# Performance work log

Measured on AMD Instinct MI355X. Metric: run time of the kernel, lower is better.

## Reference

```python
import jax, jax.numpy as jnp
import numpy as np

EMBED_DIM = 1024

def setup_inputs() -> dict:
    key = jax.random.key(0)
    kx, kwq, kbq, kwk, kbk, kwv, kbv = jax.random.split(key, 7)
    d = EMBED_DIM
    s = 1.0 / np.sqrt(d)
    x = jax.random.normal(kx, (4, 2048, d), dtype=jnp.float32)
    # nn.Linear weights are [out, in]; we store transposed [in, out] for x @ W
    Wq = jax.random.uniform(kwq, (d, d), jnp.float32, -s, s)
    bq = jax.random.uniform(kbq, (d,), jnp.float32, -s, s)
    Wk = jax.random.uniform(kwk, (d, d), jnp.float32, -s, s)
    bk = jax.random.uniform(kbk, (d,), jnp.float32, -s, s)
    Wv = jax.random.uniform(kwv, (d, d), jnp.float32, -s, s)
    bv = jax.random.uniform(kbv, (d,), jnp.float32, -s, s)
    return {"x": x, "Wq": Wq, "bq": bq, "Wk": Wk, "bk": bk, "Wv": Wv, "bv": bv}

def reference(x, Wq, bq, Wk, bk, Wv, bv):
    d = x.shape[-1]
    q = x @ Wq + bq            # [B, S, D]
    k = x @ Wk + bk            # [B, S, D]
    v = x @ Wv + bv            # [B, S, D]
    scores = jnp.einsum('bsd,btd->bst', q, k) / jnp.sqrt(jnp.asarray(d, x.dtype))
    attn = jax.nn.softmax(scores, axis=-1)  # [B, S, S]
    return jnp.einsum('bst,btd->bsd', attn, v)
```

## Files before the change

kernel.cpp:

```cpp
#include <hip/hip_runtime.h>
#include <hip/hip_bf16.h>
#include <stdint.h>


typedef short bf16x8 __attribute__((ext_vector_type(8)));
typedef float f32x4 __attribute__((ext_vector_type(4)));
typedef unsigned short us4 __attribute__((ext_vector_type(4)));
typedef unsigned short us8 __attribute__((ext_vector_type(8)));
typedef _Float16 h8v __attribute__((ext_vector_type(8)));
typedef unsigned short us;

#define B_ 4
#define S_ 2048
#define D_ 1024

__device__ __forceinline__ us f2bf(float f) {
  unsigned int u = __float_as_uint(f);
  unsigned int r = (u + 0x7fffu + ((u >> 16) & 1u)) >> 16;
  return (us)r;
}

__device__ __forceinline__ void gl2lds16(void* lds, const void* g) {
  __builtin_amdgcn_global_load_lds(
      (const __attribute__((address_space(1))) unsigned int*)(uintptr_t)g,
      (__attribute__((address_space(3))) unsigned int*)(uintptr_t)lds,
      16, 0, 0);
}

__device__ __forceinline__ void sched_fence() { __builtin_amdgcn_sched_barrier(0); }
__device__ __forceinline__ void barrier_f() {
  sched_fence(); __builtin_amdgcn_s_barrier(); sched_fence();
}

template<int BM, int R0, int R1>
__device__ __forceinline__ void stageR(us* buf, const us* gA, size_t sA,
                                       const us* gB, size_t sB,
                                       int wave, int lane) {
  int slot = ((lane & 7) ^ (lane >> 3)) << 4;
  char* l = (char*)buf;
#pragma unroll
  for (int r = R0; r < R1; ++r) {
    int row = r * 64 + wave * 8 + (lane >> 3);
    const char* src;
    if (r * 64 < BM)
      src = (const char*)gA + (size_t)row * sA + slot;
    else
      src = (const char*)gB + (size_t)(row - BM) * sB + slot;
    gl2lds16(l + r * 8192 + wave * 1024, src);
  }
}

template<int EPI, int BM, int BN, int WNS>
__global__ __launch_bounds__(512, 2) void gemm8p(
    const us* __restrict__ Aall, const us* __restrict__ Ball,
    size_t aBatch, size_t bBatch, int sAe, int sBe, int nt,
    const float* __restrict__ bq, const float* __restrict__ bk,
    const float* __restrict__ bv, void* __restrict__ outp,
    us* __restrict__ vtb) {
  __shared__ __align__(16) us lds[3][(BM + BN) * 64];
  int tid = threadIdx.x, lane = tid & 63, wave = tid >> 6;
  int wm = wave / WNS, wn = wave % WNS;
  int m0 = blockIdx.x * BM, n0 = blockIdx.y * BN;
  size_t bz = blockIdx.z;
  const us* gA = Aall + bz * aBatch + (size_t)m0 * sAe;
  const us* gB = Ball + bz * bBatch + (size_t)n0 * sBe;
  size_t sA = (size_t)sAe * 2, sB = (size_t)sBe * 2;

  stageR<BM, 0, 6>(lds[0], gA, sA, gB, sB, wave, lane);
  stageR<BM, 0, 6>(lds[1], gA + 64, sA, gB + 64, sB, wave, lane);

  int r15 = lane & 15, kg = lane >> 4, l7 = lane & 7;
  int x0 = (kg ^ l7) << 4;
  f32x4 acc[4][4] = {};

  for (int t = 0; t < nt; ++t) {
    if (t == nt - 1) asm volatile("s_waitcnt vmcnt(0)" ::: "memory");
    else             asm volatile("s_waitcnt vmcnt(6)" ::: "memory");
    barrier_f();
    const us* buf = lds[t % 3];
    us* nbuf = (us*)lds[(t + 2) % 3];
    bool dostage = (t + 2 < nt);
    const us* gA2 = gA + (size_t)(t + 2) * 64;
    const us* gB2 = gB + (size_t)(t + 2) * 64;
    const char* pa = (const char*)buf + (size_t)(wm * 64 + r15) * 128;
    const char* pb = (const char*)buf + (size_t)(BM + wn * 64 + r15) * 128;

    if (dostage) stageR<BM, 0, 3>(nbuf, gA2, sA, gB2, sB, wave, lane);
    bf16x8 A0[4], B0[4];
#pragma unroll
    for (int f = 0; f < 4; ++f) A0[f] = *(const bf16x8*)(pa + f * 2048 + x0);
#pragma unroll
    for (int f = 0; f < 4; ++f) B0[f] = *(const bf16x8*)(pb + f * 2048 + x0);
    __builtin_amdgcn_s_setprio(1);
#pragma unroll
    for (int fn = 0; fn < 4; ++fn)
#pragma unroll
      for (int fm = 0; fm < 4; ++fm)
        acc[fm][fn] = __builtin_amdgcn_mfma_f32_16x16x32_bf16(A0[fm], B0[fn], acc[fm][fn], 0, 0, 0);
    __builtin_amdgcn_s_setprio(0);

    if (dostage) stageR<BM, 3, 6>(nbuf, gA2, sA, gB2, sB, wave, lane);
    bf16x8 A1[4], B1[4];
#pragma unroll
    for (int f = 0; f < 4; ++f) A1[f] = *(const bf16x8*)(pa + f * 2048 + (x0 ^ 64));
#pragma unroll
    for (int f = 0; f < 4; ++f) B1[f] = *(const bf16x8*)(pb + f * 2048 + (x0 ^ 64));
    __builtin_amdgcn_s_setprio(1);
#pragma unroll
    for (int fn = 0; fn < 4; ++fn)
#pragma unroll
      for (int fm = 0; fm < 4; ++fm)
        acc[fm][fn] = __builtin_amdgcn_mfma_f32_16x16x32_bf16(A1[fm], B1[fn], acc[fm][fn], 0, 0, 0);
    __builtin_amdgcn_s_setprio(0);
  }

#pragma unroll
  for (int fm = 0; fm < 4; ++fm)
#pragma unroll
    for (int fn = 0; fn < 4; ++fn) {
      int col = n0 + wn * 64 + fn * 16 + r15;
      int row0 = m0 + wm * 64 + fm * 16 + ((lane >> 4) << 2);
      if constexpr (EPI == 0) {
        int mat = col >> 10;
        const float* bp = (mat == 0) ? bq : (mat == 1) ? bk : bv;
        float bb = bp[col & 1023];
        if (mat < 2) {
          us* ob = (us*)outp + ((size_t)mat << 23);
#pragma unroll
          for (int r = 0; r < 4; ++r)
            ob[(size_t)(row0 + r) * D_ + (col & 1023)] = f2bf(acc[fm][fn][r] + bb);
        } else {
          int b = row0 >> 11, trow = row0 & 2047, dcol = col & 1023;
          us4 v4 = {f2bf(acc[fm][fn][0] + bb), f2bf(acc[fm][fn][1] + bb),
                    f2bf(acc[fm][fn][2] + bb), f2bf(acc[fm][fn][3] + bb)};
          *(us4*)(vtb + (size_t)b * D_ * S_ + (size_t)dcol * S_ + trow) = v4;
        }
      } else {
        float* ob = (float*)outp + bz * (size_t)(S_ * D_);
#pragma unroll
        for (int r = 0; r < 4; ++r)
          ob[(size_t)(row0 + r) * D_ + col] = acc[fm][fn][r];
      }
    }
}

__global__ __launch_bounds__(512, 2) void s2k(
    const us* __restrict__ Aall, const us* __restrict__ Ball,
    _Float16* __restrict__ scores) {
  __shared__ __align__(16) us lds3[3][16384];
  const int tid = threadIdx.x, lane = tid & 63, wave = tid >> 6;
  const int wm = wave >> 2, wn = wave & 3;
  const int m0 = blockIdx.x * 256, n0 = blockIdx.y * 256;
  const size_t bz = blockIdx.z;
  const char* gA = (const char*)(Aall + bz * (size_t)(S_ * D_) + (size_t)m0 * D_);
  const char* gB = (const char*)(Ball + bz * (size_t)(S_ * D_) + (size_t)n0 * D_);
  const size_t sA = (size_t)D_ * 2, sB = (size_t)D_ * 2;
  const int nt = 32;

  const int r15 = lane & 15, kg = lane >> 4;
  const int srcslot = (((lane & 3) ^ ((lane >> 3) & 3)) << 4);
  const int srow = wave * 16 + (lane >> 2);

  auto stage = [&](int bi, int t) {
    char* l = (char*)lds3[bi];
    const size_t koff = (size_t)t * 64;
#pragma unroll
    for (int r = 0; r < 4; ++r) {
      int row = r * 128 + srow;
      const char* src = (row < 256)
          ? gA + (size_t)row * sA + koff + srcslot
          : gB + (size_t)(row - 256) * sB + koff + srcslot;
      gl2lds16(l + r * 8192 + wave * 1024, src);
    }
  };

  stage(0, 0);
  stage(1, 1);

  f32x4 acc[8][4] = {};
  for (int t = 0; t < nt; ++t) {
    if (t == nt - 1) asm volatile("s_waitcnt vmcnt(0)" ::: "memory");
    else             asm volatile("s_waitcnt vmcnt(4)" ::: "memory");
    barrier_f();
    if (t + 2 < nt) stage((t + 2) % 3, t + 2);
    const char* buf = (const char*)lds3[t % 3];

    bf16x8 Af[8], Bf[4];
#pragma unroll
    for (int f = 0; f < 8; ++f) {
      int tr = wm * 128 + f * 16 + r15;
      Af[f] = *(const bf16x8*)(buf + tr * 64 + ((kg ^ ((tr >> 1) & 3)) << 4));
    }
#pragma unroll
    for (int n = 0; n < 4; ++n) {
      int tr = 256 + wn * 64 + n * 16 + r15;
      Bf[n] = *(const bf16x8*)(buf + tr * 64 + ((kg ^ ((tr >> 1) & 3)) << 4));
    }
    __builtin_amdgcn_s_setprio(1);
#pragma unroll
    for (int n = 0; n < 4; ++n)
#pragma unroll
      for (int f = 0; f < 8; ++f)
        acc[f][n] = __builtin_amdgcn_mfma_f32_16x16x32_bf16(Af[f], Bf[n], acc[f][n], 0, 0, 0);
    __builtin_amdgcn_s_setprio(0);
  }

  _Float16* sc = scores + bz * (size_t)(S_ * S_);
#pragma unroll
  for (int fm = 0; fm < 8; ++fm)
#pragma unroll
    for (int fn = 0; fn < 4; ++fn) {
      int col = n0 + wn * 64 + fn * 16 + r15;
      int row0 = m0 + wm * 128 + fm * 16 + ((lane >> 4) << 2);
#pragma unroll
      for (int r = 0; r < 4; ++r)
        sc[(size_t)(row0 + r) * S_ + col] = (_Float16)(acc[fm][fn][r] * 0.03125f);
    }
}

__global__ __launch_bounds__(256) void wt_prep(const float* __restrict__ Wq,
                                               const float* __restrict__ Wk,
                                               const float* __restrict__ Wv,
                                               us* __restrict__ wtb) {
  __shared__ us hs[64][65];
  int mat = blockIdx.z;
  const float* W = (mat == 0) ? Wq : (mat == 1) ? Wk : Wv;
  int n0 = blockIdx.x * 64, k0 = blockIdx.y * 64;
  int tid = threadIdx.x;
#pragma unroll
  for (int i = 0; i < 16; ++i) {
    int idx = tid + i * 256;
    int r = idx >> 6, c = idx & 63;
    hs[r][c] = f2bf(W[(size_t)(k0 + r) * D_ + (n0 + c)]);
  }
  __syncthreads();
  us* o = wtb + ((size_t)mat << 20);
#pragma unroll
  for (int i = 0; i < 16; ++i) {
    int idx = tid + i * 256;
    int r = idx >> 6, c = idx & 63;
    o[(size_t)(n0 + r) * D_ + (k0 + c)] = hs[c][r];
  }
}

__global__ __launch_bounds__(256) void xcast(const float* __restrict__ x,
                                             us* __restrict__ xb) {
  size_t i = ((size_t)blockIdx.x * 256 + threadIdx.x) * 8;
  float4 f0 = *(const float4*)(x + i);
  float4 f1 = *(const float4*)(x + i + 4);
  float vals[8] = {f0.x, f0.y, f0.z, f0.w, f1.x, f1.y, f1.z, f1.w};
  union { bf16x8 v; us s_[8]; } H;
#pragma unroll
  for (int e = 0; e < 8; ++e) H.s_[e] = f2bf(vals[e]);
  *(bf16x8*)(xb + i) = H.v;
}

__global__ __launch_bounds__(256) void softmax_k(const _Float16* __restrict__ scores,
                                                 us* __restrict__ pb) {
  int row = blockIdx.x, tid = threadIdx.x, lane = tid & 63, wave = tid >> 6;
  const _Float16* s = scores + (size_t)row * S_;
  h8v a8 = *(const h8v*)(s + tid * 8);
  float a[8];
#pragma unroll
  for (int e = 0; e < 8; ++e) a[e] = (float)a8[e];
  float m = a[0];
#pragma unroll
  for (int e = 1; e < 8; ++e) m = fmaxf(m, a[e]);
#pragma unroll
  for (int o = 32; o; o >>= 1) m = fmaxf(m, __shfl_xor(m, o));
  __shared__ float red[4];
  if (lane == 0) red[wave] = m;
  __syncthreads();
  m = fmaxf(fmaxf(red[0], red[1]), fmaxf(red[2], red[3]));
  float p[8];
  float sum = 0.f;
#pragma unroll
  for (int e = 0; e < 8; ++e) { p[e] = expf(a[e] - m); sum += p[e]; }
#pragma unroll
  for (int o = 32; o; o >>= 1) sum += __shfl_xor(sum, o);
  __syncthreads();
  if (lane == 0) red[wave] = sum;
  __syncthreads();
  float inv = 1.0f / (red[0] + red[1] + red[2] + red[3]);
  us8 h;
#pragma unroll
  for (int e = 0; e < 8; ++e) h[e] = f2bf(p[e] * inv);
  *(us8*)(pb + (size_t)row * S_ + tid * 8) = h;
}

extern "C" void kernel_launch(void* const* d_in, const int* in_sizes, int n_in,
                              void* d_out, int out_size, void* d_ws, size_t ws_size,
                              hipStream_t stream) {
  const float* x  = (const float*)d_in[0];
  const float* Wq = (const float*)d_in[1];
  const float* bq = (const float*)d_in[2];
  const float* Wk = (const float*)d_in[3];
  const float* bk = (const float*)d_in[4];
  const float* Wv = (const float*)d_in[5];
  const float* bv = (const float*)d_in[6];
  float* out = (float*)d_out;
  char* ws = (char*)d_ws;
  const size_t MB = 1024 * 1024;
  us* qb   = (us*)(ws + 0 * MB);
  us* kb   = (us*)(ws + 16 * MB);
  us* vtb  = (us*)(ws + 32 * MB);
  us* wtb  = (us*)(ws + 48 * MB);
  us* xb   = (us*)(ws + 54 * MB);
  _Float16* scores = (_Float16*)(ws + 70 * MB);
  us* pb   = (us*)(ws + 102 * MB);

  wt_prep<<<dim3(16, 16, 3), 256, 0, stream>>>(Wq, Wk, Wv, wtb);
  xcast<<<dim3(4096), 256, 0, stream>>>(x, xb);
  gemm8p<0, 128, 256, 4><<<dim3(64, 12, 1), 512, 0, stream>>>(
      xb, wtb, 0, 0, D_, D_, 16, bq, bk, bv, qb, vtb);
  s2k<<<dim3(8, 8, 4), 512, 0, stream>>>(qb, kb, scores);
  softmax_k<<<dim3(B_ * S_), 256, 0, stream>>>(scores, pb);
  gemm8p<2, 256, 128, 2><<<dim3(8, 8, 4), 512, 0, stream>>>(
      pb, vtb, (size_t)S_ * S_, (size_t)D_ * S_, S_, S_, 32,
      nullptr, nullptr, nullptr, out, nullptr);
}
```

Measured before the change: 152.2 us.

## Fold Q and K projections into a single precomputed Wq·Wkᵀ matrix

Rewrites the scores as (x·Wq·Wkᵀ)·xᵀ plus a per-key bias c = x·(Wk·bq). Terms that are constant along a softmax row are dropped, because softmax ignores them. This removes one of the three 8192x1024x1024 projection GEMMs: one GEMM now produces E = x·M alongside the transposed V. The cost is several new small kernels: a naive MFMA product forming M from global memory, a matrix-vector pass for u, and a pass re-reading fp32 x to build c. It also adds extra bf16 rounding from storing M in bf16.

```diff
diff --git a/kernel.cpp b/kernel.cpp
--- a/kernel.cpp
+++ b/kernel.cpp
@@ -54,8 +54,7 @@
 __global__ __launch_bounds__(512, 2) void gemm8p(
     const us* __restrict__ Aall, const us* __restrict__ Ball,
     size_t aBatch, size_t bBatch, int sAe, int sBe, int nt,
-    const float* __restrict__ bq, const float* __restrict__ bk,
-    const float* __restrict__ bv, void* __restrict__ outp,
+    const float* __restrict__ bias1, void* __restrict__ outp,
     us* __restrict__ vtb) {
   __shared__ __align__(16) us lds[3][(BM + BN) * 64];
   int tid = threadIdx.x, lane = tid & 63, wave = tid >> 6;
@@ -120,16 +119,15 @@
     for (int fn = 0; fn < 4; ++fn) {
       int col = n0 + wn * 64 + fn * 16 + r15;
       int row0 = m0 + wm * 64 + fm * 16 + ((lane >> 4) << 2);
-      if constexpr (EPI == 0) {
+      if constexpr (EPI == 3) {
         int mat = col >> 10;
-        const float* bp = (mat == 0) ? bq : (mat == 1) ? bk : bv;
-        float bb = bp[col & 1023];
-        if (mat < 2) {
-          us* ob = (us*)outp + ((size_t)mat << 23);
+        if (mat == 0) {
+          us* ob = (us*)outp;
 #pragma unroll
           for (int r = 0; r < 4; ++r)
-            ob[(size_t)(row0 + r) * D_ + (col & 1023)] = f2bf(acc[fm][fn][r] + bb);
+            ob[(size_t)(row0 + r) * D_ + col] = f2bf(acc[fm][fn][r]);
         } else {
+          float bb = bias1[col & 1023];
           int b = row0 >> 11, trow = row0 & 2047, dcol = col & 1023;
           us4 v4 = {f2bf(acc[fm][fn][0] + bb), f2bf(acc[fm][fn][1] + bb),
                     f2bf(acc[fm][fn][2] + bb), f2bf(acc[fm][fn][3] + bb)};
@@ -146,7 +144,7 @@
 
 __global__ __launch_bounds__(512, 2) void s2k(
     const us* __restrict__ Aall, const us* __restrict__ Ball,
-    _Float16* __restrict__ scores) {
+    const float* __restrict__ cvp, _Float16* __restrict__ scores) {
   __shared__ __align__(16) us lds3[3][16384];
   const int tid = threadIdx.x, lane = tid & 63, wave = tid >> 6;
   const int wm = wave >> 2, wn = wave & 3;
@@ -206,25 +204,97 @@
   }
 
   _Float16* sc = scores + bz * (size_t)(S_ * S_);
+  const float* cb = cvp + bz * (size_t)S_;
 #pragma unroll
   for (int fm = 0; fm < 8; ++fm)
 #pragma unroll
     for (int fn = 0; fn < 4; ++fn) {
       int col = n0 + wn * 64 + fn * 16 + r15;
       int row0 = m0 + wm * 128 + fm * 16 + ((lane >> 4) << 2);
+      float cv = cb[col];
 #pragma unroll
       for (int r = 0; r < 4; ++r)
-        sc[(size_t)(row0 + r) * S_ + col] = (_Float16)(acc[fm][fn][r] * 0.03125f);
-    }
-}
-
-__global__ __launch_bounds__(256) void wt_prep(const float* __restrict__ Wq,
-                                               const float* __restrict__ Wk,
-                                               const float* __restrict__ Wv,
-                                               us* __restrict__ wtb) {
+        sc[(size_t)(row0 + r) * S_ + col] = (_Float16)((acc[fm][fn][r] + cv) * 0.03125f);
+    }
+}
+
+__global__ __launch_bounds__(256) void mprep(const us* __restrict__ wkb,
+                                             const us* __restrict__ wqb,
+                                             us* __restrict__ mtb) {
+  int tid = threadIdx.x, lane = tid & 63, wave = tid >> 6;
+  int j0 = blockIdx.x * 64, i0 = blockIdx.y * 64;
+  int r15 = lane & 15, kg = lane >> 4;
+  f32x4 acc[4] = {};
+  for (int kk = 0; kk < D_; kk += 32) {
+    bf16x8 a = *(const bf16x8*)(wkb + (size_t)(j0 + wave * 16 + r15) * D_ + kk + kg * 8);
+#pragma unroll
+    for (int f = 0; f < 4; ++f) {
+      bf16x8 b = *(const bf16x8*)(wqb + (size_t)(i0 + f * 16 + r15) * D_ + kk + kg * 8);
+      acc[f] = __builtin_amdgcn_mfma_f32_16x16x32_bf16(a, b, acc[f], 0, 0, 0);
+    }
+  }
+#pragma unroll
+  for (int f = 0; f < 4; ++f)
+#pragma unroll
+    for (int r = 0; r < 4; ++r)
+      mtb[(size_t)(j0 + wave * 16 + kg * 4 + r) * D_ + i0 + f * 16 + r15] = f2bf(acc[f][r]);
+}
+
+__global__ __launch_bounds__(256) void uprep(const float* __restrict__ Wk,
+                                             const float* __restrict__ bq,
+                                             float* __restrict__ u) {
+  int lane = threadIdx.x & 63, wave = threadIdx.x >> 6;
+  int i = blockIdx.x * 4 + wave;
+  const float* row = Wk + (size_t)i * D_;
+  float s = 0.f;
+#pragma unroll
+  for (int e = 0; e < 4; ++e) {
+    float4 a = *(const float4*)(row + e * 256 + lane * 4);
+    float4 b = *(const float4*)(bq + e * 256 + lane * 4);
+    s += a.x * b.x + a.y * b.y + a.z * b.z + a.w * b.w;
+  }
+#pragma unroll
+  for (int o = 32; o; o >>= 1) s += __shfl_xor(s, o);
+  if (lane == 0) u[i] = s;
+}
+
+__global__ __launch_bounds__(256) void cvec(const float* __restrict__ x,
+                                            const float* __restrict__ u,
+                                            float* __restrict__ c) {
+  int lane = threadIdx.x & 63, wave = threadIdx.x >> 6;
+  int i = blockIdx.x * 4 + wave;
+  const float* row = x + (size_t)i * D_;
+  float s = 0.f;
+#pragma unroll
+  for (int e = 0; e < 4; ++e) {
+    float4 a = *(const float4*)(row + e * 256 + lane * 4);
+    float4 b = *(const float4*)(u + e * 256 + lane * 4);
+    s += a.x * b.x + a.y * b.y + a.z * b.z + a.w * b.w;
+  }
+#pragma unroll
+  for (int o = 32; o; o >>= 1) s += __shfl_xor(s, o);
+  if (lane == 0) c[i] = s;
+}
+
+__global__ __launch_bounds__(256) void wcast(const float* __restrict__ Wq,
+                                             const float* __restrict__ Wk,
+                                             us* __restrict__ wqb,
+                                             us* __restrict__ wkb) {
+  size_t i = ((size_t)blockIdx.x * 256 + threadIdx.x) * 8;
+  const float* src = blockIdx.y ? Wk : Wq;
+  us* dst = blockIdx.y ? wkb : wqb;
+  float4 f0 = *(const float4*)(src + i);
+  float4 f1 = *(const float4*)(src + i + 4);
+  float vals[8] = {f0.x, f0.y, f0.z, f0.w, f1.x, f1.y, f1.z, f1.w};
+  union { bf16x8 v; us s_[8]; } H;
+#pragma unroll
+  for (int e = 0; e < 8; ++e) H.s_[e] = f2bf(vals[e]);
+  *(bf16x8*)(dst + i) = H.v;
+}
+
+__global__ __launch_bounds__(256) void wtv(const float* __restrict__ W,
+                                           us* __restrict__ o) {
   __shared__ us hs[64][65];
-  int mat = blockIdx.z;
-  const float* W = (mat == 0) ? Wq : (mat == 1) ? Wk : Wv;
   int n0 = blockIdx.x * 64, k0 = blockIdx.y * 64;
   int tid = threadIdx.x;
 #pragma unroll
@@ -234,7 +304,6 @@
     hs[r][c] = f2bf(W[(size_t)(k0 + r) * D_ + (n0 + c)]);
   }
   __syncthreads();
-  us* o = wtb + ((size_t)mat << 20);
 #pragma unroll
   for (int i = 0; i < 16; ++i) {
     int idx = tid + i * 256;
@@ -298,24 +367,33 @@
   const float* bk = (const float*)d_in[4];
   const float* Wv = (const float*)d_in[5];
   const float* bv = (const float*)d_in[6];
+  (void)bk;
   float* out = (float*)d_out;
   char* ws = (char*)d_ws;
   const size_t MB = 1024 * 1024;
-  us* qb   = (us*)(ws + 0 * MB);
-  us* kb   = (us*)(ws + 16 * MB);
+  us* eb   = (us*)(ws + 0 * MB);
+  us* wqb  = (us*)(ws + 16 * MB);
+  us* wkb  = (us*)(ws + 18 * MB);
+  float* u = (float*)(ws + 20 * MB);
+  float* c = (float*)(ws + 21 * MB);
   us* vtb  = (us*)(ws + 32 * MB);
-  us* wtb  = (us*)(ws + 48 * MB);
+  us* mtb  = (us*)(ws + 48 * MB);
+  us* wvt  = (us*)(ws + 50 * MB);
   us* xb   = (us*)(ws + 54 * MB);
   _Float16* scores = (_Float16*)(ws + 70 * MB);
   us* pb   = (us*)(ws + 102 * MB);
 
-  wt_prep<<<dim3(16, 16, 3), 256, 0, stream>>>(Wq, Wk, Wv, wtb);
+  wcast<<<dim3(512, 2), 256, 0, stream>>>(Wq, Wk, wqb, wkb);
+  wtv<<<dim3(16, 16), 256, 0, stream>>>(Wv, wvt);
   xcast<<<dim3(4096), 256, 0, stream>>>(x, xb);
-  gemm8p<0, 128, 256, 4><<<dim3(64, 12, 1), 512, 0, stream>>>(
-      xb, wtb, 0, 0, D_, D_, 16, bq, bk, bv, qb, vtb);
-  s2k<<<dim3(8, 8, 4), 512, 0, stream>>>(qb, kb, scores);
+  mprep<<<dim3(16, 16), 256, 0, stream>>>(wkb, wqb, mtb);
+  uprep<<<dim3(256), 256, 0, stream>>>(Wk, bq, u);
+  cvec<<<dim3(2048), 256, 0, stream>>>(x, u, c);
+  gemm8p<3, 128, 256, 4><<<dim3(64, 8, 1), 512, 0, stream>>>(
+      xb, mtb, 0, 0, D_, D_, 16, bv, eb, vtb);
+  s2k<<<dim3(8, 8, 4), 512, 0, stream>>>(eb, xb, c, scores);
   softmax_k<<<dim3(B_ * S_), 256, 0, stream>>>(scores, pb);
   gemm8p<2, 256, 128, 2><<<dim3(8, 8, 4), 512, 0, stream>>>(
       pb, vtb, (size_t)S_ * S_, (size_t)D_ * S_, S_, S_, 32,
-      nullptr, nullptr, nullptr, out, nullptr);
-}
+      nullptr, out, nullptr);
+}
```

Result: slower. 167.2 us (+9.9%).
